# Kernel tuning notes

Hardware: AMD Instinct MI355X
Metric: run time of the kernel (lower is better)

## Reference

```python
import jax, jax.numpy as jnp
import numpy as np

B = 2048; E = 6; H = 4; D = 128; DH = D // H
LTXT = 24; CS = 20; JD = 7; SD = 16; LD = 32; K = 2
NLB = 4; NLD = 3; VOCAB = 512; DFF = 4 * D


def _ln(x, s, b, eps=1e-5):
    m = x.mean(-1, keepdims=True)
    v = ((x - m) ** 2).mean(-1, keepdims=True)
    return (x - m) * jax.lax.rsqrt(v + eps) * s + b


def _mha(xq, xkv, Wqkv, bqkv, Wo, bo, key_pad=None):
    # torch nn.MultiheadAttention, batch_first, eval (no dropout)
    Wq, Wk, Wv = jnp.split(Wqkv, 3, axis=-1)
    bq, bk, bv = jnp.split(bqkv, 3)
    Bc, Lq, _ = xq.shape
    Lk = xkv.shape[1]
    q = (xq @ Wq + bq).reshape(Bc, Lq, H, DH)
    k = (xkv @ Wk + bk).reshape(Bc, Lk, H, DH)
    v = (xkv @ Wv + bv).reshape(Bc, Lk, H, DH)
    s = jnp.einsum('bqhd,bkhd->bhqk', q, k) * (1.0 / DH ** 0.5)
    if key_pad is not None:
        s = jnp.where(key_pad[:, None, None, :], -1e9, s)
    a = jax.nn.softmax(s, axis=-1)
    o = jnp.einsum('bhqk,bkhd->bqhd', a, v).reshape(Bc, Lq, D)
    return o @ Wo + bo


def _sinusoidal_pe(L, d):
    pos = jnp.arange(L, dtype=jnp.float32)[:, None]
    div = jnp.exp(jnp.arange(0, d, 2, dtype=jnp.float32) * (-np.log(10000.0) / d))
    pe = jnp.zeros((L, d), jnp.float32)
    pe = pe.at[:, 0::2].set(jnp.sin(pos * div))
    return pe.at[:, 1::2].set(jnp.cos(pos * div))


def _forward(ids, state, tok_emb, pos_emb, bert_Wqkv, bert_bqkv, bert_Wo, bert_bo, bert_W1, bert_b1, bert_W2, bert_b2, bert_ln_s, bert_ln_b, bert_lnf_s, bert_lnf_b, se_W1, se_b1, se_W2, se_b2, se_ln_s, se_ln_b, r_W1, r_b1, r_W2, r_b2, r_ln_s, r_ln_b, gate_W, gate_b, exp_sp_W, exp_sp_b, exp_zp_W, exp_zp_b, exp_attn_Wqkv, exp_attn_bqkv, exp_attn_Wo, exp_attn_bo, exp_ln_s, exp_ln_b, exp_ff_W1, exp_ff_b1, exp_ff_W2, exp_ff_b2, exp_head_W, exp_head_b):
    Bc = ids.shape[0]
    gelu = lambda t: jax.nn.gelu(t, approximate=False)
    # ---- MiniBERT (post-LN encoder) ----
    pad = ids == 0  # PAD token
    x = tok_emb[ids] + pos_emb[None]  # [B,24,128]
    for l in range(NLB):
        a = _mha(x, x, bert_Wqkv[l], bert_bqkv[l], bert_Wo[l], bert_bo[l], pad)
        x = _ln(x + a, bert_ln_s[l, 0], bert_ln_b[l, 0])
        h = gelu(x @ bert_W1[l] + bert_b1[l]) @ bert_W2[l] + bert_b2[l]
        x = _ln(x + h, bert_ln_s[l, 1], bert_ln_b[l, 1])
    intent = _ln(x, bert_lnf_s, bert_lnf_b)[:, 0]  # CLS embedding [B,128]
    # ---- StateEncoder (MLP + LN) ----
    semb = _ln(gelu(state @ se_W1 + se_b1) @ se_W2 + se_b2, se_ln_s, se_ln_b)
    # ---- FusionRouter: top-k gating ----
    fused = _ln(gelu(jnp.concatenate([intent, semb], -1) @ r_W1 + r_b1) @ r_W2 + r_b2, r_ln_s, r_ln_b)
    logits = fused @ gate_W + gate_b  # [B,6]
    all_probs = jax.nn.softmax(logits, axis=-1)
    tv, ti = jax.lax.top_k(logits, K)
    weights = jax.nn.softmax(tv, axis=-1)  # [B,2]
    # ---- ACTExperts, inference path (z = 0) ----
    qpe = _sinusoidal_pe(CS, D)
    z = jnp.zeros((Bc, LD), state.dtype)

    def one_expert(sp_W, sp_b, zp_W, zp_b, aW, ab, oW, ob, lns, lnb, fW1, fb1, fW2, fb2, hW, hb):
        mem = jnp.stack([state @ sp_W + sp_b, z @ zp_W + zp_b], axis=1)  # [B,2,128]
        xq = jnp.broadcast_to(qpe[None], (Bc, CS, D))
        for l in range(NLD):  # norm_first decoder layers, relu FFN
            xn = _ln(xq, lns[l, 0], lnb[l, 0])
            xq = xq + _mha(xn, xn, aW[l, 0], ab[l, 0], oW[l, 0], ob[l, 0])
            xn = _ln(xq, lns[l, 1], lnb[l, 1])
            xq = xq + _mha(xn, mem, aW[l, 1], ab[l, 1], oW[l, 1], ob[l, 1])
            xn = _ln(xq, lns[l, 2], lnb[l, 2])
            xq = xq + jax.nn.relu(xn @ fW1[l] + fb1[l]) @ fW2[l] + fb2[l]
        return xq @ hW + hb  # [B,20,7]

    outs = jax.vmap(one_expert)(exp_sp_W, exp_sp_b, exp_zp_W, exp_zp_b, exp_attn_Wqkv, exp_attn_bqkv, exp_attn_Wo, exp_attn_bo, exp_ln_s, exp_ln_b, exp_ff_W1, exp_ff_b1, exp_ff_W2, exp_ff_b2, exp_head_W, exp_head_b)  # [E,B,20,7]
    # scatter top-k weights to a dense [B,E] gate and combine expert outputs
    w_full = jnp.zeros((Bc, E), logits.dtype).at[jnp.arange(Bc)[:, None], ti].add(weights)
    return jnp.einsum('be,ebtj->btj', w_full, outs)


def setup_inputs() -> dict:
    key = jax.random.key(0)
    it = iter(jax.random.split(key, 64))
    w = lambda *shape: jax.random.normal(next(it), shape, jnp.float32) * 0.05
    inp = {}
    inp['ids'] = jax.random.randint(next(it), (B, LTXT), 0, VOCAB, dtype=jnp.int32)
    inp['state'] = jax.random.normal(next(it), (B, SD), jnp.float32)
    inp['tok_emb'] = w(VOCAB, D).at[0].set(0.0)  # padding_idx=0
    inp['pos_emb'] = w(LTXT, D)
    inp['bert_Wqkv'] = w(NLB, D, 3 * D); inp['bert_bqkv'] = jnp.zeros((NLB, 3 * D))
    inp['bert_Wo'] = w(NLB, D, D); inp['bert_bo'] = jnp.zeros((NLB, D))
    inp['bert_W1'] = w(NLB, D, DFF); inp['bert_b1'] = jnp.zeros((NLB, DFF))
    inp['bert_W2'] = w(NLB, DFF, D); inp['bert_b2'] = jnp.zeros((NLB, D))
    inp['bert_ln_s'] = jnp.ones((NLB, 2, D)); inp['bert_ln_b'] = jnp.zeros((NLB, 2, D))
    inp['bert_lnf_s'] = jnp.ones((D,)); inp['bert_lnf_b'] = jnp.zeros((D,))
    inp['se_W1'] = w(SD, D); inp['se_b1'] = jnp.zeros((D,))
    inp['se_W2'] = w(D, D); inp['se_b2'] = jnp.zeros((D,))
    inp['se_ln_s'] = jnp.ones((D,)); inp['se_ln_b'] = jnp.zeros((D,))
    inp['r_W1'] = w(2 * D, D); inp['r_b1'] = jnp.zeros((D,))
    inp['r_W2'] = w(D, D); inp['r_b2'] = jnp.zeros((D,))
    inp['r_ln_s'] = jnp.ones((D,)); inp['r_ln_b'] = jnp.zeros((D,))
    inp['gate_W'] = w(D, E) * 10.0  # non-degenerate routing (source inits zeros)
    inp['gate_b'] = jnp.zeros((E,))
    inp['exp_sp_W'] = w(E, SD, D); inp['exp_sp_b'] = jnp.zeros((E, D))
    inp['exp_zp_W'] = w(E, LD, D); inp['exp_zp_b'] = jnp.zeros((E, D))
    inp['exp_attn_Wqkv'] = w(E, NLD, 2, D, 3 * D); inp['exp_attn_bqkv'] = jnp.zeros((E, NLD, 2, 3 * D))
    inp['exp_attn_Wo'] = w(E, NLD, 2, D, D); inp['exp_attn_bo'] = jnp.zeros((E, NLD, 2, D))
    inp['exp_ln_s'] = jnp.ones((E, NLD, 3, D)); inp['exp_ln_b'] = jnp.zeros((E, NLD, 3, D))
    inp['exp_ff_W1'] = w(E, NLD, D, DFF); inp['exp_ff_b1'] = jnp.zeros((E, NLD, DFF))
    inp['exp_ff_W2'] = w(E, NLD, DFF, D); inp['exp_ff_b2'] = jnp.zeros((E, NLD, D))
    inp['exp_head_W'] = w(E, D, JD); inp['exp_head_b'] = jnp.zeros((E, JD))
    return inp


def reference(ids, state, tok_emb, pos_emb, bert_Wqkv, bert_bqkv, bert_Wo, bert_bo, bert_W1, bert_b1, bert_W2, bert_b2, bert_ln_s, bert_ln_b, bert_lnf_s, bert_lnf_b, se_W1, se_b1, se_W2, se_b2, se_ln_s, se_ln_b, r_W1, r_b1, r_W2, r_b2, r_ln_s, r_ln_b, gate_W, gate_b, exp_sp_W, exp_sp_b, exp_zp_W, exp_zp_b, exp_attn_Wqkv, exp_attn_bqkv, exp_attn_Wo, exp_attn_bo, exp_ln_s, exp_ln_b, exp_ff_W1, exp_ff_b1, exp_ff_W2, exp_ff_b2, exp_head_W, exp_head_b):
    return _forward(ids, state, tok_emb, pos_emb, bert_Wqkv, bert_bqkv, bert_Wo, bert_bo, bert_W1, bert_b1, bert_W2, bert_b2, bert_ln_s, bert_ln_b, bert_lnf_s, bert_lnf_b, se_W1, se_b1, se_W2, se_b2, se_ln_s, se_ln_b, r_W1, r_b1, r_W2, r_b2, r_ln_s, r_ln_b, gate_W, gate_b, exp_sp_W, exp_sp_b, exp_zp_W, exp_zp_b, exp_attn_Wqkv, exp_attn_bqkv, exp_attn_Wo, exp_attn_bo, exp_ln_s, exp_ln_b, exp_ff_W1, exp_ff_b1, exp_ff_W2, exp_ff_b2, exp_head_W, exp_head_b)
```

## Files before the change

kernel.cpp:

```cpp
#include <hip/hip_runtime.h>
#include <math.h>

#define DEVI __device__ __forceinline__

namespace {

constexpr int Bn   = 2048;
constexpr int En   = 6;
constexpr int Hn   = 4;
constexpr int Dn   = 128;
constexpr int DHn  = 32;
constexpr int LTn  = 24;
constexpr int CSn  = 20;
constexpr int JDn  = 7;
constexpr int SDn  = 16;
constexpr int NLBn = 4;
constexpr int NLDn = 3;
constexpr int DFFn = 512;
constexpr float INV_SQRT_DH = 0.17677669529663687f;

constexpr int PAIRS  = 4096;
constexpr int MPMAX  = PAIRS * 20 + En * 128;
constexpr int NBGMAX = PAIRS * 20 / 128 + En;
constexpr int GEXP_OFF = 64;
constexpr int GMT_OFF  = 64 + NBGMAX;

constexpr int ROWSB = Bn * LTn;

constexpr int HSTR = 36;

typedef float f32x4v __attribute__((ext_vector_type(4)));
typedef short short8 __attribute__((ext_vector_type(8)));

DEVI float geluf(float x) { return 0.5f * x * (1.0f + erff(x * 0.70710678118654752f)); }

DEVI short f2bf(float f) {
  unsigned u = __float_as_uint(f);
  return (short)((u + 0x7FFFu + ((u >> 16) & 1u)) >> 16);
}
DEVI float bf2f(short s) { return __uint_as_float(((unsigned)(unsigned short)s) << 16); }
DEVI void split2(float v, short& h, short& l) {
  h = f2bf(v);
  l = f2bf(v - bf2f(h));
}

DEVI size_t apos(int row, int col, int KT) {
  return (((size_t)(row >> 4) * KT + (col >> 5)) * 64 + ((col >> 3) & 3) * 16 + (row & 15)) * 8
         + (col & 7);
}

DEVI size_t hpos(int rl, int col) {
  return (((size_t)((rl >> 4) * 16 + (col >> 5)) * 64) + ((col >> 3) & 3) * 16 + (rl & 15)) * 8
         + (col & 7);
}

__global__ void pack_kernel(const float* __restrict__ W, short* __restrict__ out,
                            const int K, const int N, const int total)
{
  const int p = (int)blockIdx.x * 256 + (int)threadIdx.x;
  if (p >= total) return;
  const int perMat = (K * N) >> 3;
  const int m = p / perMat, r = p - m * perMat;
  const int t = r >> 6, lane = r & 63;
  const int KT = K >> 5;
  const int nt = t / KT, kt = t - nt * KT;
  const int row0 = kt * 32 + (lane >> 4) * 8;
  const int col  = nt * 16 + (lane & 15);
  const float* src = W + (size_t)m * K * N;
  short8 v;
#pragma unroll
  for (int j = 0; j < 8; ++j) v[j] = f2bf(src[(size_t)(row0 + j) * N + col]);
  *reinterpret_cast<short8*>(out + (size_t)p * 8) = v;
}

__global__ void pack2_kernel(const float* __restrict__ W, short* __restrict__ out,
                             const int K, const int N, const int total)
{
  const int p = (int)blockIdx.x * 256 + (int)threadIdx.x;
  if (p >= total) return;
  const int perMat = (K * N) >> 3;
  const int m = p / perMat, r = p - m * perMat;
  const int t = r >> 6, lane = r & 63;
  const int KT = K >> 5;
  const int nt = t / KT, kt = t - nt * KT;
  const int row0 = kt * 32 + (lane >> 4) * 8;
  const int col  = nt * 16 + (lane & 15);
  const float* src = W + (size_t)m * K * N;
  short8 vh, vl;
// ... 117 lines not shown
    }
    acc *= INV_SQRT_DH;
    if (pad_s[j]) acc = -1e9f;
    att[e] = acc;
  }
  __syncthreads();
  if (tid < 2 * LTn) {
    const int r = tid >> 1, h0 = (tid & 1) * 12;
    float* row = att + r * LTn + h0;
    float m = row[0];
#pragma unroll
    for (int j = 1; j < 12; ++j) m = fmaxf(m, row[j]);
    m = fmaxf(m, __shfl_xor(m, 1));
    float s = 0.f;
#pragma unroll
    for (int j = 0; j < 12; ++j) { const float ex = expf(row[j] - m); row[j] = ex; s += ex; }
    s += __shfl_xor(s, 1);
    if ((tid & 1) == 0) inv[r] = 1.f / s;
  }
  __syncthreads();
  for (int e = tid; e < LTn * 32; e += 64) {
    const int i = e >> 5, c = e & 31;
    const float* arow = att + i * LTn;
    float acc = 0.f;
#pragma unroll 4
    for (int j = 0; j < LTn; ++j) acc = fmaf(arow[j], vs[j * HSTR + c], acc);
    acc *= inv[i];
    short hh, ll; split2(acc, hh, ll);
    const size_t pk = apos(row0 + i, h * 32 + c, 4);
    Ah[pk] = hh; Al[pk] = ll;
  }
}

__global__ __launch_bounds__(256) void bo_ln_kernel(
    const short* __restrict__ Ah, const short* __restrict__ Al,
    const short* __restrict__ Bp, const float* __restrict__ bo,
    const float* __restrict__ gs, const float* __restrict__ gb,
    float* __restrict__ X, short* __restrict__ OAh, short* __restrict__ OAl)
{
  __shared__ float red[16][4][2];
  const int mt0 = (int)blockIdx.x * 4;
  const int lane = (int)threadIdx.x & 63, wv = (int)threadIdx.x >> 6;
  const int r0 = lane & 15, g = lane >> 4;
  short8 bh[2][4], bl[2][4];
#pragma unroll
  for (int i = 0; i < 2; ++i)
#pragma unroll
    for (int kt = 0; kt < 4; ++kt) {
      const short* tb = Bp + (((size_t)(wv * 2 + i) * 4 + kt) << 10);
      bh[i][kt] = *reinterpret_cast<const short8*>(tb + lane * 8);
      bl[i][kt] = *reinterpret_cast<const short8*>(tb + 512 + lane * 8);
    }
  for (int mt = 0; mt < 4; ++mt) {
    const int mtg = mt0 + mt;
    short8 ah[4], al[4];
#pragma unroll
    for (int kt = 0; kt < 4; ++kt) {
      ah[kt] = *reinterpret_cast<const short8*>(Ah + (((size_t)mtg * 4 + kt) * 64 + lane) * 8);
      al[kt] = *reinterpret_cast<const short8*>(Al + (((size_t)mtg * 4 + kt) * 64 + lane) * 8);
    }
    float v[2][4];
#pragma unroll
    for (int i = 0; i < 2; ++i) {
      f32x4v c = {0.f, 0.f, 0.f, 0.f};
#pragma unroll
      for (int kt = 0; kt < 4; ++kt) {
        c = __builtin_amdgcn_mfma_f32_16x16x32_bf16(ah[kt], bh[i][kt], c, 0, 0, 0);
        c = __builtin_amdgcn_mfma_f32_16x16x32_bf16(al[kt], bh[i][kt], c, 0, 0, 0);
        c = __builtin_amdgcn_mfma_f32_16x16x32_bf16(ah[kt], bl[i][kt], c, 0, 0, 0);
      }
      const int col = (wv * 2 + i) * 16 + r0;
      const float bb = bo[col];
#pragma unroll
      for (int q = 0; q < 4; ++q) {
        const int row = mtg * 16 + g * 4 + q;
        v[i][q] = c[q] + bb + X[(size_t)row * 128 + col];
      }
    }
    float s1[4], s2[4];
#pragma unroll
    for (int q = 0; q < 4; ++q) {
      s1[q] = v[0][q] + v[1][q];
      s2[q] = v[0][q] * v[0][q] + v[1][q] * v[1][q];
    }
#pragma unroll
    for (int o = 1; o < 16; o <<= 1)
#pragma unroll
      for (int q = 0; q < 4; ++q) { s1[q] += __shfl_xor(s1[q], o); s2[q] += __shfl_xor(s2[q], o); }
    if (r0 == 0)
#pragma unroll
      for (int q = 0; q < 4; ++q) { red[g * 4 + q][wv][0] = s1[q]; red[g * 4 + q][wv][1] = s2[q]; }
    __syncthreads();
#pragma unroll
    for (int q = 0; q < 4; ++q) {
      const int r = g * 4 + q;
      const float t1 = red[r][0][0] + red[r][1][0] + red[r][2][0] + red[r][3][0];
      const float t2 = red[r][0][1] + red[r][1][1] + red[r][2][1] + red[r][3][1];
      const float m  = t1 * (1.f / 128.f);
      const float rs = rsqrtf(t2 * (1.f / 128.f) - m * m + 1e-5f);
      const int row = mtg * 16 + r;
#pragma unroll
      for (int i = 0; i < 2; ++i) {
        const int col = (wv * 2 + i) * 16 + r0;
        const float o = (v[i][q] - m) * rs * gs[col] + gb[col];
        X[(size_t)row * 128 + col] = o;
        short hh, ll; split2(o, hh, ll);
        const size_t pk = apos(row, col, 4);
        OAh[pk] = hh; OAl[pk] = ll;
      }
    }
    __syncthreads();
  }
}

__global__ __launch_bounds__(512) void bffn_kernel(
    const short* __restrict__ Ah, const short* __restrict__ Al,
    const short* __restrict__ W1p, const short* __restrict__ W2p,
    const float* __restrict__ b1, const float* __restrict__ b2,
    const float* __restrict__ gs, const float* __restrict__ gb,
    float* __restrict__ X, short* __restrict__ OAh, short* __restrict__ OAl)
{
  __shared__ short HhL[2 * 16 * 64 * 8];
  __shared__ short HlL[2 * 16 * 64 * 8];
  __shared__ float red[16][8][2];
  const int mtg0 = (int)blockIdx.x * 2;
  const int lane = (int)threadIdx.x & 63, wv = (int)threadIdx.x >> 6;
  const int r0 = lane & 15, g = lane >> 4;
  short8 ah[2][4], al[2][4];
#pragma unroll
  for (int mtl = 0; mtl < 2; ++mtl)
#pragma unroll
    for (int kt = 0; kt < 4; ++kt) {
      ah[mtl][kt] = *reinterpret_cast<const short8*>(
          Ah + (((size_t)(mtg0 + mtl) * 4 + kt) * 64 + lane) * 8);
      al[mtl][kt] = *reinterpret_cast<const short8*>(
          Al + (((size_t)(mtg0 + mtl) * 4 + kt) * 64 + lane) * 8);
    }
#pragma unroll
  for (int i = 0; i < 4; ++i) {
    const int nt = wv * 4 + i;
    short8 bh[4], bl[4];
#pragma unroll
    for (int kt = 0; kt < 4; ++kt) {
      const short* tb = W1p + (((size_t)(nt * 4 + kt)) << 10);
      bh[kt] = *reinterpret_cast<const short8*>(tb + lane * 8);
      bl[kt] = *reinterpret_cast<const short8*>(tb + 512 + lane * 8);
    }
    const int col = nt * 16 + r0;
    const float bb = b1[col];
#pragma unroll
    for (int mtl = 0; mtl < 2; ++mtl) {
      f32x4v c = {0.f, 0.f, 0.f, 0.f};
#pragma unroll
      for (int kt = 0; kt < 4; ++kt) {
        c = __builtin_amdgcn_mfma_f32_16x16x32_bf16(ah[mtl][kt], bh[kt], c, 0, 0, 0);
        c = __builtin_amdgcn_mfma_f32_16x16x32_bf16(al[mtl][kt], bh[kt], c, 0, 0, 0);
        c = __builtin_amdgcn_mfma_f32_16x16x32_bf16(ah[mtl][kt], bl[kt], c, 0, 0, 0);
      }
#pragma unroll
      for (int q = 0; q < 4; ++q) {
        const int rl = mtl * 16 + g * 4 + q;
        short hh, ll; split2(geluf(c[q] + bb), hh, ll);
        const size_t hp = hpos(rl, col);
        HhL[hp] = hh; HlL[hp] = ll;
      }
    }
  }
  __syncthreads();
  const int col = wv * 16 + r0;
  f32x4v c2[2];
#pragma unroll
  for (int mtl = 0; mtl < 2; ++mtl) c2[mtl] = (f32x4v){0.f, 0.f, 0.f, 0.f};
#pragma unroll
  for (int kk = 0; kk < 16; ++kk) {
    const short* tb = W2p + (((size_t)(wv * 16 + kk)) << 10);
    const short8 b2h = *reinterpret_cast<const short8*>(tb + lane * 8);
    const short8 b2l = *reinterpret_cast<const short8*>(tb + 512 + lane * 8);
#pragma unroll
    for (int mtl = 0; mtl < 2; ++mtl) {
      const size_t ap = (((size_t)(mtl * 16 + kk) * 64 + lane)) * 8;
      const short8 a2h = *reinterpret_cast<const short8*>(HhL + ap);
      const short8 a2l = *reinterpret_cast<const short8*>(HlL + ap);
      c2[mtl] = __builtin_amdgcn_mfma_f32_16x16x32_bf16(a2h, b2h, c2[mtl], 0, 0, 0);
      c2[mtl] = __builtin_amdgcn_mfma_f32_16x16x32_bf16(a2l, b2h, c2[mtl], 0, 0, 0);
      c2[mtl] = __builtin_amdgcn_mfma_f32_16x16x32_bf16(a2h, b2l, c2[mtl], 0, 0, 0);
    }
  }
  const float bb2 = b2[col];
  for (int mtl = 0; mtl < 2; ++mtl) {
    const int mtg = mtg0 + mtl;
    float v[4], s1[4], s2[4];
#pragma unroll
    for (int q = 0; q < 4; ++q) {
      const int row = mtg * 16 + g * 4 + q;
      v[q] = c2[mtl][q] + bb2 + X[(size_t)row * 128 + col];
      s1[q] = v[q]; s2[q] = v[q] * v[q];
    }
#pragma unroll
    for (int o = 1; o < 16; o <<= 1)
#pragma unroll
      for (int q = 0; q < 4; ++q) { s1[q] += __shfl_xor(s1[q], o); s2[q] += __shfl_xor(s2[q], o); }
    if (r0 == 0)
#pragma unroll
      for (int q = 0; q < 4; ++q) { red[g * 4 + q][wv][0] = s1[q]; red[g * 4 + q][wv][1] = s2[q]; }
    __syncthreads();
#pragma unroll
    for (int q = 0; q < 4; ++q) {
      const int r = g * 4 + q;
      float t1 = 0.f, t2 = 0.f;
#pragma unroll
      for (int w = 0; w < 8; ++w) { t1 += red[r][w][0]; t2 += red[r][w][1]; }
      const float m  = t1 * (1.f / 128.f);
      const float rs = rsqrtf(t2 * (1.f / 128.f) - m * m + 1e-5f);
      const int row = mtg * 16 + r;
      const float o = (v[q] - m) * rs * gs[col] + gb[col];
      X[(size_t)row * 128 + col] = o;
      short hh, ll; split2(o, hh, ll);
      const size_t pk = apos(row, col, 4);
      OAh[pk] = hh; OAl[pk] = ll;
    }
    __syncthreads();
  }
}

__global__ __launch_bounds__(256) void bintent_kernel(
    const float* __restrict__ X, const float* __restrict__ lnf_s,
    const float* __restrict__ lnf_b, float* __restrict__ intent)
{
  const int w = (int)threadIdx.x >> 6, lane = (int)threadIdx.x & 63;
  const int b = (int)blockIdx.x * 4 + w;
  const float* xr = X + (size_t)b * LTn * 128;
  const float a0 = xr[lane], a1 = xr[lane + 64];
  float s1 = a0 + a1, s2 = a0 * a0 + a1 * a1;
#pragma unroll
  for (int o = 32; o > 0; o >>= 1) { s1 += __shfl_xor(s1, o); s2 += __shfl_xor(s2, o); }
  const float m  = s1 * (1.f / 128.f);
  const float rs = rsqrtf(s2 * (1.f / 128.f) - m * m + 1e-5f);
  intent[b * 128 + lane]      = (a0 - m) * rs * lnf_s[lane]      + lnf_b[lane];
  intent[b * 128 + lane + 64] = (a1 - m) * rs * lnf_s[lane + 64] + lnf_b[lane + 64];
}

struct RouterP {
  const float* state; const float* intent;
  const float* se_W1; const float* se_b1; const float* se_W2; const float* se_b2;
  const float* se_ln_s; const float* se_ln_b;
  const float* r_W1; const float* r_b1; const float* r_W2; const float* r_b2;
  const float* r_ln_s; const float* r_ln_b;
  const float* gate_W; const float* gate_b;
// ... 278 lines not shown
        for (int q = 0; q < 4; ++q) { red[g * 4 + q][wv][0] = s1[q]; red[g * 4 + q][wv][1] = s2[q]; }
      __syncthreads();
#pragma unroll
      for (int q = 0; q < 4; ++q) {
        const int r = g * 4 + q;
        const float t1 = red[r][0][0] + red[r][1][0] + red[r][2][0] + red[r][3][0];
        const float t2 = red[r][0][1] + red[r][1][1] + red[r][2][1] + red[r][3][1];
        const float m  = t1 * (1.f / 128.f);
        const float rs = rsqrtf(t2 * (1.f / 128.f) - m * m + 1e-5f);
        const int row = (mt0 + mt) * 16 + r;
#pragma unroll
        for (int i = 0; i < 2; ++i) {
          const int col = (wv * 2 + i) * 16 + r0;
          const float o = (v[i][q] - m) * rs * gs[col] + gb[col];
          X[(size_t)row * 128 + col] = v[i][q];
          OutP[apos(row, col, 4)] = f2bf(o);
        }
      }
      __syncthreads();
    }
  }
}

template<bool DOLN>
__global__ __launch_bounds__(512) void effn_kernel(
    const short* __restrict__ A, const short* __restrict__ W1b, const int strideW1,
    const float* __restrict__ b1b, const int strideB1,
    const short* __restrict__ W2b, const int strideW2,
    const float* __restrict__ b2b, const int strideB2,
    float* __restrict__ X, short* __restrict__ OutP,
    const float* __restrict__ lnsA, const float* __restrict__ lnbA, const int subOff,
    const int* __restrict__ sch)
{
  __shared__ short HsL[4 * 16 * 64 * 8];
  __shared__ float red[16][8][2];
  const int k = (int)blockIdx.x;
  if (k >= sch[0]) return;
  const int ex  = sch[GEXP_OFF + k];
  const int mt0 = sch[GMT_OFF + k] + (int)blockIdx.y * 4;
  const short* W1p = W1b + (size_t)ex * strideW1;
  const short* W2p = W2b + (size_t)ex * strideW2;
  const float* b1 = b1b + (size_t)ex * strideB1;
  const float* b2 = b2b + (size_t)ex * strideB2;
  const float* gs = DOLN ? lnsA + ex * (NLDn * 3 * 128) + subOff : nullptr;
  const float* gb = DOLN ? lnbA + ex * (NLDn * 3 * 128) + subOff : nullptr;
  const int lane = (int)threadIdx.x & 63, wv = (int)threadIdx.x >> 6;
  const int r0 = lane & 15, g = lane >> 4;
  short8 a[4][4];
#pragma unroll
  for (int mtl = 0; mtl < 4; ++mtl)
#pragma unroll
    for (int kt = 0; kt < 4; ++kt)
      a[mtl][kt] = *reinterpret_cast<const short8*>(
          A + (((size_t)(mt0 + mtl) * 4 + kt) * 64 + lane) * 8);
#pragma unroll
  for (int i = 0; i < 4; ++i) {
    const int nt = wv * 4 + i;
    short8 bw[4];
#pragma unroll
    for (int kt = 0; kt < 4; ++kt)
      bw[kt] = *reinterpret_cast<const short8*>(
          W1p + (((size_t)(nt * 4 + kt) * 64 + lane)) * 8);
    const int col = nt * 16 + r0;
    const float bb = b1[col];
#pragma unroll
    for (int mtl = 0; mtl < 4; ++mtl) {
      f32x4v c = {0.f, 0.f, 0.f, 0.f};
#pragma unroll
      for (int kt = 0; kt < 4; ++kt)
        c = __builtin_amdgcn_mfma_f32_16x16x32_bf16(a[mtl][kt], bw[kt], c, 0, 0, 0);
#pragma unroll
      for (int q = 0; q < 4; ++q) {
        const int rl = mtl * 16 + g * 4 + q;
        HsL[hpos(rl, col)] = f2bf(fmaxf(c[q] + bb, 0.f));
      }
    }
  }
  __syncthreads();
  const int col = wv * 16 + r0;
  f32x4v c2[4];
#pragma unroll
  for (int mtl = 0; mtl < 4; ++mtl) c2[mtl] = (f32x4v){0.f, 0.f, 0.f, 0.f};
#pragma unroll
  for (int kk = 0; kk < 16; ++kk) {
    const short8 bw = *reinterpret_cast<const short8*>(
        W2p + (((size_t)(wv * 16 + kk) * 64 + lane)) * 8);
#pragma unroll
    for (int mtl = 0; mtl < 4; ++mtl) {
      const short8 aw = *reinterpret_cast<const short8*>(
          HsL + (((size_t)(mtl * 16 + kk) * 64 + lane)) * 8);
      c2[mtl] = __builtin_amdgcn_mfma_f32_16x16x32_bf16(aw, bw, c2[mtl], 0, 0, 0);
    }
  }
  const float bb2 = b2[col];
  for (int mtl = 0; mtl < 4; ++mtl) {
    const int mtg = mt0 + mtl;
    float v[4];
#pragma unroll
    for (int q = 0; q < 4; ++q) {
      const int row = mtg * 16 + g * 4 + q;
      v[q] = c2[mtl][q] + bb2 + X[(size_t)row * 128 + col];
    }
    if (DOLN) {
      float s1[4], s2[4];
#pragma unroll
      for (int q = 0; q < 4; ++q) { s1[q] = v[q]; s2[q] = v[q] * v[q]; }
#pragma unroll
      for (int o = 1; o < 16; o <<= 1)
#pragma unroll
        for (int q = 0; q < 4; ++q) { s1[q] += __shfl_xor(s1[q], o); s2[q] += __shfl_xor(s2[q], o); }
      if (r0 == 0)
#pragma unroll
        for (int q = 0; q < 4; ++q) { red[g * 4 + q][wv][0] = s1[q]; red[g * 4 + q][wv][1] = s2[q]; }
      __syncthreads();
#pragma unroll
      for (int q = 0; q < 4; ++q) {
        const int r = g * 4 + q;
        float t1 = 0.f, t2 = 0.f;
#pragma unroll
        for (int w = 0; w < 8; ++w) { t1 += red[r][w][0]; t2 += red[r][w][1]; }
        const float m  = t1 * (1.f / 128.f);
        const float rs = rsqrtf(t2 * (1.f / 128.f) - m * m + 1e-5f);
        const int row = mtg * 16 + r;
        const float o = (v[q] - m) * rs * gs[col] + gb[col];
        X[(size_t)row * 128 + col] = v[q];
        OutP[apos(row, col, 4)] = f2bf(o);
// ... 249 lines not shown
    pack_kernel<<<dim3((t2c + 255) / 256), dim3(256), 0, stream>>>(
        (const float*)d_in[42], pF2, 512, 128, t2c);
    const int bq = 4 * 6144;
    pack2_kernel<<<dim3((bq + 255) / 256), dim3(256), 0, stream>>>(
        (const float*)d_in[4], pbQ, 128, 384, bq);
    const int bo = 4 * 2048;
    pack2_kernel<<<dim3((bo + 255) / 256), dim3(256), 0, stream>>>(
        (const float*)d_in[6], pbO, 128, 128, bo);
    const int bw1 = 4 * 8192;
    pack2_kernel<<<dim3((bw1 + 255) / 256), dim3(256), 0, stream>>>(
        (const float*)d_in[8], pbW1, 128, 512, bw1);
    const int bw2 = 4 * 8192;
    pack2_kernel<<<dim3((bw2 + 255) / 256), dim3(256), 0, stream>>>(
        (const float*)d_in[10], pbW2, 512, 128, bw2);
    compose_kernel<<<dim3(En * NLDn), dim3(256), 0, stream>>>(
        (const float*)d_in[30], (const float*)d_in[31], (const float*)d_in[33],
        (const float*)d_in[34], (const float*)d_in[35], Cmat, k0c, k1c);
  }

  {
    const float* bq  = (const float*)d_in[5];
    const float* bo  = (const float*)d_in[7];
    const float* b1  = (const float*)d_in[9];
    const float* b2  = (const float*)d_in[11];
    const float* lns = (const float*)d_in[12];
    const float* lnb = (const float*)d_in[13];

    bembed_kernel<<<dim3(ROWSB / 16), dim3(256), 0, stream>>>(
        ids, tok_emb, pos_emb, Xb, Ah, Al);
    for (int l = 0; l < NLBn; ++l) {
      bqkv_kernel<<<dim3(ROWSB / 64, 3), dim3(256), 0, stream>>>(
          Ah, Al, pbQ + (size_t)l * 98304, bq + l * 384, SBb);
      battn_kernel<<<dim3(Bn, Hn), dim3(64), 0, stream>>>(SBb, ids, Ah, Al);
      bo_ln_kernel<<<dim3(ROWSB / 64), dim3(256), 0, stream>>>(
          Ah, Al, pbO + (size_t)l * 32768, bo + l * 128,
          lns + l * 256, lnb + l * 256, Xb, Ah, Al);
      bffn_kernel<<<dim3(ROWSB / 32), dim3(512), 0, stream>>>(
          Ah, Al, pbW1 + (size_t)l * 131072, pbW2 + (size_t)l * 131072,
          b1 + l * 512, b2 + l * 128,
          lns + l * 256 + 128, lnb + l * 256 + 128, Xb, Ah, Al);
    }
    bintent_kernel<<<dim3(Bn / 4), dim3(256), 0, stream>>>(
        Xb, (const float*)d_in[14], (const float*)d_in[15], intent);
  }

  {
    RouterP rp;
    rp.state = state; rp.intent = intent;
    rp.se_W1 = (const float*)d_in[16]; rp.se_b1 = (const float*)d_in[17];
    rp.se_W2 = (const float*)d_in[18]; rp.se_b2 = (const float*)d_in[19];
    rp.se_ln_s = (const float*)d_in[20]; rp.se_ln_b = (const float*)d_in[21];
    rp.r_W1 = (const float*)d_in[22]; rp.r_b1 = (const float*)d_in[23];
    rp.r_W2 = (const float*)d_in[24]; rp.r_b2 = (const float*)d_in[25];
    rp.r_ln_s = (const float*)d_in[26]; rp.r_ln_b = (const float*)d_in[27];
    rp.gate_W = (const float*)d_in[28]; rp.gate_b = (const float*)d_in[29];
    rp.ridx = ridx; rp.rwgt = rwgt;
    router_kernel<<<dim3(Bn), dim3(128), 0, stream>>>(rp);
  }

  const float* ab   = (const float*)d_in[35];
  const float* abo  = (const float*)d_in[37];
  const float* lnsA = (const float*)d_in[38];
  const float* lnbA = (const float*)d_in[39];
  const float* fb1A = (const float*)d_in[41];
  const float* fb2A = (const float*)d_in[43];
  const float* hW   = (const float*)d_in[44];
  const float* hB   = (const float*)d_in[45];

  {
    sched_kernel<<<dim3(1), dim3(256), 0, stream>>>(ridx, sch, plist, prow, pexp, ppos);
    xinit_kernel<<<dim3(MPMAX * 32 / 256), dim3(256), 0, stream>>>(qpe, sch, X2);
    ln_pack_kernel<<<dim3(MPMAX / 16), dim3(256), 0, stream>>>(
        X2, ANP, lnsA, lnbA, 0, sch);
// ... 39 lines not shown
```

Before: 1.410 ms.

## Fuse attention output projection, LayerNorm and FFN into one BERT kernel

Merges the output-projection+LayerNorm kernel and the FFN+LayerNorm kernel into a single 512-thread kernel per 32-row tile. The normalized attention output is kept in LDS as a bf16 hi/lo split instead of round-tripping through global X and the packed A buffers. The FFN hidden layer is computed in two halves to fit LDS, which adds extra barriers. This removes one launch per layer and a global write/read of the intermediate activations. The second residual is now rebuilt from the split bf16 copy, giving a slightly different rounding path.

```diff
diff --git a/kernel.cpp b/kernel.cpp
--- a/kernel.cpp
+++ b/kernel.cpp
@@ -54,6 +54,11 @@
          + (col & 7);
 }
 
+DEVI size_t hposh(int rl, int col) {
+  return (((size_t)((rl >> 4) * 8 + (col >> 5)) * 64) + ((col >> 3) & 3) * 16 + (rl & 15)) * 8
+         + (col & 7);
+}
+
 __global__ void pack_kernel(const float* __restrict__ W, short* __restrict__ out,
                             const int K, const int N, const int total)
 {
@@ -237,168 +242,151 @@
   }
 }
 
-__global__ __launch_bounds__(256) void bo_ln_kernel(
+__global__ __launch_bounds__(512) void bfused_kernel(
     const short* __restrict__ Ah, const short* __restrict__ Al,
-    const short* __restrict__ Bp, const float* __restrict__ bo,
-    const float* __restrict__ gs, const float* __restrict__ gb,
-    float* __restrict__ X, short* __restrict__ OAh, short* __restrict__ OAl)
-{
-  __shared__ float red[16][4][2];
-  const int mt0 = (int)blockIdx.x * 4;
-  const int lane = (int)threadIdx.x & 63, wv = (int)threadIdx.x >> 6;
-  const int r0 = lane & 15, g = lane >> 4;
-  short8 bh[2][4], bl[2][4];
-#pragma unroll
-  for (int i = 0; i < 2; ++i)
-#pragma unroll
-    for (int kt = 0; kt < 4; ++kt) {
-      const short* tb = Bp + (((size_t)(wv * 2 + i) * 4 + kt) << 10);
-      bh[i][kt] = *reinterpret_cast<const short8*>(tb + lane * 8);
-      bl[i][kt] = *reinterpret_cast<const short8*>(tb + 512 + lane * 8);
-    }
-  for (int mt = 0; mt < 4; ++mt) {
-    const int mtg = mt0 + mt;
-    short8 ah[4], al[4];
-#pragma unroll
-    for (int kt = 0; kt < 4; ++kt) {
-      ah[kt] = *reinterpret_cast<const short8*>(Ah + (((size_t)mtg * 4 + kt) * 64 + lane) * 8);
-      al[kt] = *reinterpret_cast<const short8*>(Al + (((size_t)mtg * 4 + kt) * 64 + lane) * 8);
-    }
-    float v[2][4];
-#pragma unroll
-    for (int i = 0; i < 2; ++i) {
-      f32x4v c = {0.f, 0.f, 0.f, 0.f};
-#pragma unroll
-      for (int kt = 0; kt < 4; ++kt) {
-        c = __builtin_amdgcn_mfma_f32_16x16x32_bf16(ah[kt], bh[i][kt], c, 0, 0, 0);
-        c = __builtin_amdgcn_mfma_f32_16x16x32_bf16(al[kt], bh[i][kt], c, 0, 0, 0);
-        c = __builtin_amdgcn_mfma_f32_16x16x32_bf16(ah[kt], bl[i][kt], c, 0, 0, 0);
-      }
-      const int col = (wv * 2 + i) * 16 + r0;
-      const float bb = bo[col];
-#pragma unroll
-      for (int q = 0; q < 4; ++q) {
-        const int row = mtg * 16 + g * 4 + q;
-        v[i][q] = c[q] + bb + X[(size_t)row * 128 + col];
-      }
-    }
-    float s1[4], s2[4];
-#pragma unroll
-    for (int q = 0; q < 4; ++q) {
-      s1[q] = v[0][q] + v[1][q];
-      s2[q] = v[0][q] * v[0][q] + v[1][q] * v[1][q];
-    }
-#pragma unroll
-    for (int o = 1; o < 16; o <<= 1)
-#pragma unroll
-      for (int q = 0; q < 4; ++q) { s1[q] += __shfl_xor(s1[q], o); s2[q] += __shfl_xor(s2[q], o); }
-    if (r0 == 0)
-#pragma unroll
-      for (int q = 0; q < 4; ++q) { red[g * 4 + q][wv][0] = s1[q]; red[g * 4 + q][wv][1] = s2[q]; }
-    __syncthreads();
-#pragma unroll
-    for (int q = 0; q < 4; ++q) {
-      const int r = g * 4 + q;
-      const float t1 = red[r][0][0] + red[r][1][0] + red[r][2][0] + red[r][3][0];
-      const float t2 = red[r][0][1] + red[r][1][1] + red[r][2][1] + red[r][3][1];
-      const float m  = t1 * (1.f / 128.f);
-      const float rs = rsqrtf(t2 * (1.f / 128.f) - m * m + 1e-5f);
-      const int row = mtg * 16 + r;
-#pragma unroll
-      for (int i = 0; i < 2; ++i) {
-        const int col = (wv * 2 + i) * 16 + r0;
-        const float o = (v[i][q] - m) * rs * gs[col] + gb[col];
-        X[(size_t)row * 128 + col] = o;
-        short hh, ll; split2(o, hh, ll);
-        const size_t pk = apos(row, col, 4);
-        OAh[pk] = hh; OAl[pk] = ll;
-      }
-    }
-    __syncthreads();
-  }
-}
-
-__global__ __launch_bounds__(512) void bffn_kernel(
-    const short* __restrict__ Ah, const short* __restrict__ Al,
+    const short* __restrict__ Op, const float* __restrict__ bo,
+    const float* __restrict__ gs1, const float* __restrict__ gb1,
     const short* __restrict__ W1p, const short* __restrict__ W2p,
     const float* __restrict__ b1, const float* __restrict__ b2,
-    const float* __restrict__ gs, const float* __restrict__ gb,
+    const float* __restrict__ gs2, const float* __restrict__ gb2,
     float* __restrict__ X, short* __restrict__ OAh, short* __restrict__ OAl)
 {
-  __shared__ short HhL[2 * 16 * 64 * 8];
-  __shared__ short HlL[2 * 16 * 64 * 8];
+  __shared__ short AhL[2 * 4 * 64 * 8];
+  __shared__ short AlL[2 * 4 * 64 * 8];
+  __shared__ short HhL[2 * 8 * 64 * 8];
+  __shared__ short HlL[2 * 8 * 64 * 8];
   __shared__ float red[16][8][2];
   const int mtg0 = (int)blockIdx.x * 2;
   const int lane = (int)threadIdx.x & 63, wv = (int)threadIdx.x >> 6;
   const int r0 = lane & 15, g = lane >> 4;
-  short8 ah[2][4], al[2][4];
-#pragma unroll
-  for (int mtl = 0; mtl < 2; ++mtl)
+  const int col = wv * 16 + r0;
+
+  float vA[2][4];
+  {
+    short8 obh[4], obl[4];
 #pragma unroll
     for (int kt = 0; kt < 4; ++kt) {
-      ah[mtl][kt] = *reinterpret_cast<const short8*>(
-          Ah + (((size_t)(mtg0 + mtl) * 4 + kt) * 64 + lane) * 8);
-      al[mtl][kt] = *reinterpret_cast<const short8*>(
-          Al + (((size_t)(mtg0 + mtl) * 4 + kt) * 64 + lane) * 8);
-    }
-#pragma unroll
-  for (int i = 0; i < 4; ++i) {
-    const int nt = wv * 4 + i;
-    short8 bh[4], bl[4];
-#pragma unroll
-    for (int kt = 0; kt < 4; ++kt) {
-      const short* tb = W1p + (((size_t)(nt * 4 + kt)) << 10);
-      bh[kt] = *reinterpret_cast<const short8*>(tb + lane * 8);
-      bl[kt] = *reinterpret_cast<const short8*>(tb + 512 + lane * 8);
-    }
-    const int col = nt * 16 + r0;
-    const float bb = b1[col];
+      const short* tb = Op + (((size_t)(wv * 4 + kt)) << 10);
+      obh[kt] = *reinterpret_cast<const short8*>(tb + lane * 8);
+      obl[kt] = *reinterpret_cast<const short8*>(tb + 512 + lane * 8);
+    }
+    const float bbo = bo[col];
 #pragma unroll
     for (int mtl = 0; mtl < 2; ++mtl) {
+      const int mtg = mtg0 + mtl;
       f32x4v c = {0.f, 0.f, 0.f, 0.f};
 #pragma unroll
       for (int kt = 0; kt < 4; ++kt) {
-        c = __builtin_amdgcn_mfma_f32_16x16x32_bf16(ah[mtl][kt], bh[kt], c, 0, 0, 0);
-        c = __builtin_amdgcn_mfma_f32_16x16x32_bf16(al[mtl][kt], bh[kt], c, 0, 0, 0);
-        c = __builtin_amdgcn_mfma_f32_16x16x32_bf16(ah[mtl][kt], bl[kt], c, 0, 0, 0);
+        const short8 ah = *reinterpret_cast<const short8*>(
+            Ah + (((size_t)mtg * 4 + kt) * 64 + lane) * 8);
+        const short8 al = *reinterpret_cast<const short8*>(
+            Al + (((size_t)mtg * 4 + kt) * 64 + lane) * 8);
+        c = __builtin_amdgcn_mfma_f32_16x16x32_bf16(ah, obh[kt], c, 0, 0, 0);
+        c = __builtin_amdgcn_mfma_f32_16x16x32_bf16(al, obh[kt], c, 0, 0, 0);
+        c = __builtin_amdgcn_mfma_f32_16x16x32_bf16(ah, obl[kt], c, 0, 0, 0);
       }
 #pragma unroll
       for (int q = 0; q < 4; ++q) {
-        const int rl = mtl * 16 + g * 4 + q;
-        short hh, ll; split2(geluf(c[q] + bb), hh, ll);
-        const size_t hp = hpos(rl, col);
-        HhL[hp] = hh; HlL[hp] = ll;
-      }
-    }
-  }
-  __syncthreads();
-  const int col = wv * 16 + r0;
+        const int row = mtg * 16 + g * 4 + q;
+        vA[mtl][q] = c[q] + bbo + X[(size_t)row * 128 + col];
+      }
+    }
+  }
+  for (int mtl = 0; mtl < 2; ++mtl) {
+    float s1[4], s2[4];
+#pragma unroll
+    for (int q = 0; q < 4; ++q) { s1[q] = vA[mtl][q]; s2[q] = vA[mtl][q] * vA[mtl][q]; }
+#pragma unroll
+    for (int o = 1; o < 16; o <<= 1)
+#pragma unroll
+      for (int q = 0; q < 4; ++q) { s1[q] += __shfl_xor(s1[q], o); s2[q] += __shfl_xor(s2[q], o); }
+    if (r0 == 0)
+#pragma unroll
+      for (int q = 0; q < 4; ++q) { red[g * 4 + q][wv][0] = s1[q]; red[g * 4 + q][wv][1] = s2[q]; }
+    __syncthreads();
+#pragma unroll
+    for (int q = 0; q < 4; ++q) {
+      const int r = g * 4 + q;
+      float t1 = 0.f, t2 = 0.f;
+#pragma unroll
+      for (int w = 0; w < 8; ++w) { t1 += red[r][w][0]; t2 += red[r][w][1]; }
+      const float m  = t1 * (1.f / 128.f);
+      const float rs = rsqrtf(t2 * (1.f / 128.f) - m * m + 1e-5f);
+      const float o = (vA[mtl][q] - m) * rs * gs1[col] + gb1[col];
+      short hh, ll; split2(o, hh, ll);
+      const size_t pk = apos(mtl * 16 + r, col, 4);
+      AhL[pk] = hh; AlL[pk] = ll;
+    }
+    __syncthreads();
+  }
+
   f32x4v c2[2];
 #pragma unroll
   for (int mtl = 0; mtl < 2; ++mtl) c2[mtl] = (f32x4v){0.f, 0.f, 0.f, 0.f};
-#pragma unroll
-  for (int kk = 0; kk < 16; ++kk) {
-    const short* tb = W2p + (((size_t)(wv * 16 + kk)) << 10);
-    const short8 b2h = *reinterpret_cast<const short8*>(tb + lane * 8);
-    const short8 b2l = *reinterpret_cast<const short8*>(tb + 512 + lane * 8);
-#pragma unroll
-    for (int mtl = 0; mtl < 2; ++mtl) {
-      const size_t ap = (((size_t)(mtl * 16 + kk) * 64 + lane)) * 8;
-      const short8 a2h = *reinterpret_cast<const short8*>(HhL + ap);
-      const short8 a2l = *reinterpret_cast<const short8*>(HlL + ap);
-      c2[mtl] = __builtin_amdgcn_mfma_f32_16x16x32_bf16(a2h, b2h, c2[mtl], 0, 0, 0);
-      c2[mtl] = __builtin_amdgcn_mfma_f32_16x16x32_bf16(a2l, b2h, c2[mtl], 0, 0, 0);
-      c2[mtl] = __builtin_amdgcn_mfma_f32_16x16x32_bf16(a2h, b2l, c2[mtl], 0, 0, 0);
-    }
-  }
+  for (int half = 0; half < 2; ++half) {
+    if (half) __syncthreads();
+#pragma unroll
+    for (int i = 0; i < 2; ++i) {
+      const int ntl = wv * 2 + i;
+      const int ntg = half * 16 + ntl;
+      short8 bh[4], bl[4];
+#pragma unroll
+      for (int kt = 0; kt < 4; ++kt) {
+        const short* tb = W1p + (((size_t)(ntg * 4 + kt)) << 10);
+        bh[kt] = *reinterpret_cast<const short8*>(tb + lane * 8);
+        bl[kt] = *reinterpret_cast<const short8*>(tb + 512 + lane * 8);
+      }
+      const int colh = ntl * 16 + r0;
+      const float bb = b1[ntg * 16 + r0];
+#pragma unroll
+      for (int mtl = 0; mtl < 2; ++mtl) {
+        f32x4v c = {0.f, 0.f, 0.f, 0.f};
+#pragma unroll
+        for (int kt = 0; kt < 4; ++kt) {
+          const size_t ap = (((size_t)(mtl * 4 + kt) * 64 + lane)) * 8;
+          const short8 a2h = *reinterpret_cast<const short8*>(AhL + ap);
+          const short8 a2l = *reinterpret_cast<const short8*>(AlL + ap);
+          c = __builtin_amdgcn_mfma_f32_16x16x32_bf16(a2h, bh[kt], c, 0, 0, 0);
+          c = __builtin_amdgcn_mfma_f32_16x16x32_bf16(a2l, bh[kt], c, 0, 0, 0);
+          c = __builtin_amdgcn_mfma_f32_16x16x32_bf16(a2h, bl[kt], c, 0, 0, 0);
+        }
+#pragma unroll
+        for (int q = 0; q < 4; ++q) {
+          const int rl = mtl * 16 + g * 4 + q;
+          short hh, ll; split2(geluf(c[q] + bb), hh, ll);
+          const size_t hp = hposh(rl, colh);
+          HhL[hp] = hh; HlL[hp] = ll;
+        }
+      }
+    }
+    __syncthreads();
+#pragma unroll
+    for (int kk = 0; kk < 8; ++kk) {
+      const int kkg = half * 8 + kk;
+      const short* tb = W2p + (((size_t)(wv * 16 + kkg)) << 10);
+      const short8 b2h = *reinterpret_cast<const short8*>(tb + lane * 8);
+      const short8 b2l = *reinterpret_cast<const short8*>(tb + 512 + lane * 8);
+#pragma unroll
+      for (int mtl = 0; mtl < 2; ++mtl) {
+        const size_t ap = (((size_t)(mtl * 8 + kk) * 64 + lane)) * 8;
+        const short8 a2h = *reinterpret_cast<const short8*>(HhL + ap);
+        const short8 a2l = *reinterpret_cast<const short8*>(HlL + ap);
+        c2[mtl] = __builtin_amdgcn_mfma_f32_16x16x32_bf16(a2h, b2h, c2[mtl], 0, 0, 0);
+        c2[mtl] = __builtin_amdgcn_mfma_f32_16x16x32_bf16(a2l, b2h, c2[mtl], 0, 0, 0);
+        c2[mtl] = __builtin_amdgcn_mfma_f32_16x16x32_bf16(a2h, b2l, c2[mtl], 0, 0, 0);
+      }
+    }
+  }
+  __syncthreads();
   const float bb2 = b2[col];
   for (int mtl = 0; mtl < 2; ++mtl) {
     const int mtg = mtg0 + mtl;
     float v[4], s1[4], s2[4];
 #pragma unroll
     for (int q = 0; q < 4; ++q) {
-      const int row = mtg * 16 + g * 4 + q;
-      v[q] = c2[mtl][q] + bb2 + X[(size_t)row * 128 + col];
+      const size_t pk = apos(mtl * 16 + g * 4 + q, col, 4);
+      const float oatt = bf2f(AhL[pk]) + bf2f(AlL[pk]);
+      v[q] = c2[mtl][q] + bb2 + oatt;
       s1[q] = v[q]; s2[q] = v[q] * v[q];
     }
 #pragma unroll
@@ -418,7 +406,7 @@
       const float m  = t1 * (1.f / 128.f);
       const float rs = rsqrtf(t2 * (1.f / 128.f) - m * m + 1e-5f);
       const int row = mtg * 16 + r;
-      const float o = (v[q] - m) * rs * gs[col] + gb[col];
+      const float o = (v[q] - m) * rs * gs2[col] + gb2[col];
       X[(size_t)row * 128 + col] = o;
       short hh, ll; split2(o, hh, ll);
       const size_t pk = apos(row, col, 4);
@@ -1138,13 +1126,13 @@
       bqkv_kernel<<<dim3(ROWSB / 64, 3), dim3(256), 0, stream>>>(
           Ah, Al, pbQ + (size_t)l * 98304, bq + l * 384, SBb);
       battn_kernel<<<dim3(Bn, Hn), dim3(64), 0, stream>>>(SBb, ids, Ah, Al);
-      bo_ln_kernel<<<dim3(ROWSB / 64), dim3(256), 0, stream>>>(
+      bfused_kernel<<<dim3(ROWSB / 32), dim3(512), 0, stream>>>(
           Ah, Al, pbO + (size_t)l * 32768, bo + l * 128,
-          lns + l * 256, lnb + l * 256, Xb, Ah, Al);
-      bffn_kernel<<<dim3(ROWSB / 32), dim3(512), 0, stream>>>(
-          Ah, Al, pbW1 + (size_t)l * 131072, pbW2 + (size_t)l * 131072,
+          lns + l * 256, lnb + l * 256,
+          pbW1 + (size_t)l * 131072, pbW2 + (size_t)l * 131072,
           b1 + l * 512, b2 + l * 128,
-          lns + l * 256 + 128, lnb + l * 256 + 128, Xb, Ah, Al);
+          lns + l * 256 + 128, lnb + l * 256 + 128,
+          Xb, Ah, Al);
     }
     bintent_kernel<<<dim3(Bn / 4), dim3(256), 0, stream>>>(
         Xb, (const float*)d_in[14], (const float*)d_in[15], intent);
```

Result: slower. 1.520 ms (+7.8%).

## Split FFN hidden dimension into two halves to halve LDS footprint

Applied to the files above, without the earlier changes.

Both the BERT FFN and expert FFN kernels now process the 512-wide hidden layer in two 256-wide halves. Each half computes its GELU/ReLU activations into shared memory, then immediately accumulates the second GEMM over that half. This halves the LDS buffers, which can let more blocks reside per CU. The cost is an extra barrier per half and reloading the A fragments once per half.

```diff
diff --git a/kernel.cpp b/kernel.cpp
--- a/kernel.cpp
+++ b/kernel.cpp
@@ -49,8 +49,8 @@
          + (col & 7);
 }
 
-DEVI size_t hpos(int rl, int col) {
-  return (((size_t)((rl >> 4) * 16 + (col >> 5)) * 64) + ((col >> 3) & 3) * 16 + (rl & 15)) * 8
+DEVI size_t hposh(int rl, int col) {
+  return (((size_t)((rl >> 4) * 8 + (col >> 5)) * 64) + ((col >> 3) & 3) * 16 + (rl & 15)) * 8
          + (col & 7);
 }
 
@@ -325,72 +325,80 @@
     const float* __restrict__ gs, const float* __restrict__ gb,
     float* __restrict__ X, short* __restrict__ OAh, short* __restrict__ OAl)
 {
-  __shared__ short HhL[2 * 16 * 64 * 8];
-  __shared__ short HlL[2 * 16 * 64 * 8];
+  __shared__ short HhL[2 * 8 * 64 * 8];
+  __shared__ short HlL[2 * 8 * 64 * 8];
   __shared__ float red[16][8][2];
   const int mtg0 = (int)blockIdx.x * 2;
   const int lane = (int)threadIdx.x & 63, wv = (int)threadIdx.x >> 6;
   const int r0 = lane & 15, g = lane >> 4;
-  short8 ah[2][4], al[2][4];
-#pragma unroll
-  for (int mtl = 0; mtl < 2; ++mtl)
-#pragma unroll
-    for (int kt = 0; kt < 4; ++kt) {
-      ah[mtl][kt] = *reinterpret_cast<const short8*>(
-          Ah + (((size_t)(mtg0 + mtl) * 4 + kt) * 64 + lane) * 8);
-      al[mtl][kt] = *reinterpret_cast<const short8*>(
-          Al + (((size_t)(mtg0 + mtl) * 4 + kt) * 64 + lane) * 8);
-    }
-#pragma unroll
-  for (int i = 0; i < 4; ++i) {
-    const int nt = wv * 4 + i;
-    short8 bh[4], bl[4];
-#pragma unroll
-    for (int kt = 0; kt < 4; ++kt) {
-      const short* tb = W1p + (((size_t)(nt * 4 + kt)) << 10);
-      bh[kt] = *reinterpret_cast<const short8*>(tb + lane * 8);
-      bl[kt] = *reinterpret_cast<const short8*>(tb + 512 + lane * 8);
-    }
-    const int col = nt * 16 + r0;
-    const float bb = b1[col];
-#pragma unroll
-    for (int mtl = 0; mtl < 2; ++mtl) {
-      f32x4v c = {0.f, 0.f, 0.f, 0.f};
-#pragma unroll
-      for (int kt = 0; kt < 4; ++kt) {
-        c = __builtin_amdgcn_mfma_f32_16x16x32_bf16(ah[mtl][kt], bh[kt], c, 0, 0, 0);
-        c = __builtin_amdgcn_mfma_f32_16x16x32_bf16(al[mtl][kt], bh[kt], c, 0, 0, 0);
-        c = __builtin_amdgcn_mfma_f32_16x16x32_bf16(ah[mtl][kt], bl[kt], c, 0, 0, 0);
-      }
-#pragma unroll
-      for (int q = 0; q < 4; ++q) {
-        const int rl = mtl * 16 + g * 4 + q;
-        short hh, ll; split2(geluf(c[q] + bb), hh, ll);
-        const size_t hp = hpos(rl, col);
-        HhL[hp] = hh; HlL[hp] = ll;
-      }
-    }
-  }
-  __syncthreads();
+  f32x4v c2[2];
+  c2[0] = (f32x4v){0.f, 0.f, 0.f, 0.f};
+  c2[1] = (f32x4v){0.f, 0.f, 0.f, 0.f};
+#pragma unroll 1
+  for (int half = 0; half < 2; ++half) {
+    if (half) __syncthreads();
+    {
+      short8 ah[2][4], al[2][4];
+#pragma unroll
+      for (int mtl = 0; mtl < 2; ++mtl)
+#pragma unroll
+        for (int kt = 0; kt < 4; ++kt) {
+          ah[mtl][kt] = *reinterpret_cast<const short8*>(
+              Ah + (((size_t)(mtg0 + mtl) * 4 + kt) * 64 + lane) * 8);
+          al[mtl][kt] = *reinterpret_cast<const short8*>(
+              Al + (((size_t)(mtg0 + mtl) * 4 + kt) * 64 + lane) * 8);
+        }
+#pragma unroll
+      for (int i = 0; i < 2; ++i) {
+        const int ntl = wv * 2 + i;
+        const int ntg = half * 16 + ntl;
+        short8 bh[4], bl[4];
+#pragma unroll
+        for (int kt = 0; kt < 4; ++kt) {
+          const short* tb = W1p + (((size_t)(ntg * 4 + kt)) << 10);
+          bh[kt] = *reinterpret_cast<const short8*>(tb + lane * 8);
+          bl[kt] = *reinterpret_cast<const short8*>(tb + 512 + lane * 8);
+        }
+        const int colh = ntl * 16 + r0;
+        const float bb = b1[ntg * 16 + r0];
+#pragma unroll
+        for (int mtl = 0; mtl < 2; ++mtl) {
+          f32x4v c = {0.f, 0.f, 0.f, 0.f};
+#pragma unroll
+          for (int kt = 0; kt < 4; ++kt) {
+            c = __builtin_amdgcn_mfma_f32_16x16x32_bf16(ah[mtl][kt], bh[kt], c, 0, 0, 0);
+            c = __builtin_amdgcn_mfma_f32_16x16x32_bf16(al[mtl][kt], bh[kt], c, 0, 0, 0);
+            c = __builtin_amdgcn_mfma_f32_16x16x32_bf16(ah[mtl][kt], bl[kt], c, 0, 0, 0);
+          }
+#pragma unroll
+          for (int q = 0; q < 4; ++q) {
+            const int rl = mtl * 16 + g * 4 + q;
+            short hh, ll; split2(geluf(c[q] + bb), hh, ll);
+            const size_t hp = hposh(rl, colh);
+            HhL[hp] = hh; HlL[hp] = ll;
+          }
+        }
+      }
+    }
+    __syncthreads();
+#pragma unroll
+    for (int kk = 0; kk < 8; ++kk) {
+      const int kkg = half * 8 + kk;
+      const short* tb = W2p + (((size_t)(wv * 16 + kkg)) << 10);
+      const short8 b2h = *reinterpret_cast<const short8*>(tb + lane * 8);
+      const short8 b2l = *reinterpret_cast<const short8*>(tb + 512 + lane * 8);
+#pragma unroll
+      for (int mtl = 0; mtl < 2; ++mtl) {
+        const size_t ap = (((size_t)(mtl * 8 + kk) * 64 + lane)) * 8;
+        const short8 a2h = *reinterpret_cast<const short8*>(HhL + ap);
+        const short8 a2l = *reinterpret_cast<const short8*>(HlL + ap);
+        c2[mtl] = __builtin_amdgcn_mfma_f32_16x16x32_bf16(a2h, b2h, c2[mtl], 0, 0, 0);
+        c2[mtl] = __builtin_amdgcn_mfma_f32_16x16x32_bf16(a2l, b2h, c2[mtl], 0, 0, 0);
+        c2[mtl] = __builtin_amdgcn_mfma_f32_16x16x32_bf16(a2h, b2l, c2[mtl], 0, 0, 0);
+      }
+    }
+  }
   const int col = wv * 16 + r0;
-  f32x4v c2[2];
-#pragma unroll
-  for (int mtl = 0; mtl < 2; ++mtl) c2[mtl] = (f32x4v){0.f, 0.f, 0.f, 0.f};
-#pragma unroll
-  for (int kk = 0; kk < 16; ++kk) {
-    const short* tb = W2p + (((size_t)(wv * 16 + kk)) << 10);
-    const short8 b2h = *reinterpret_cast<const short8*>(tb + lane * 8);
-    const short8 b2l = *reinterpret_cast<const short8*>(tb + 512 + lane * 8);
-#pragma unroll
-    for (int mtl = 0; mtl < 2; ++mtl) {
-      const size_t ap = (((size_t)(mtl * 16 + kk) * 64 + lane)) * 8;
-      const short8 a2h = *reinterpret_cast<const short8*>(HhL + ap);
-      const short8 a2l = *reinterpret_cast<const short8*>(HlL + ap);
-      c2[mtl] = __builtin_amdgcn_mfma_f32_16x16x32_bf16(a2h, b2h, c2[mtl], 0, 0, 0);
-      c2[mtl] = __builtin_amdgcn_mfma_f32_16x16x32_bf16(a2l, b2h, c2[mtl], 0, 0, 0);
-      c2[mtl] = __builtin_amdgcn_mfma_f32_16x16x32_bf16(a2h, b2l, c2[mtl], 0, 0, 0);
-    }
-  }
   const float bb2 = b2[col];
   for (int mtl = 0; mtl < 2; ++mtl) {
     const int mtg = mtg0 + mtl;
@@ -763,7 +771,7 @@
     const float* __restrict__ lnsA, const float* __restrict__ lnbA, const int subOff,
     const int* __restrict__ sch)
 {
-  __shared__ short HsL[4 * 16 * 64 * 8];
+  __shared__ short HsL[4 * 8 * 64 * 8];
   __shared__ float red[16][8][2];
   const int k = (int)blockIdx.x;
   if (k >= sch[0]) return;
@@ -777,52 +785,60 @@
   const float* gb = DOLN ? lnbA + ex * (NLDn * 3 * 128) + subOff : nullptr;
   const int lane = (int)threadIdx.x & 63, wv = (int)threadIdx.x >> 6;
   const int r0 = lane & 15, g = lane >> 4;
-  short8 a[4][4];
-#pragma unroll
-  for (int mtl = 0; mtl < 4; ++mtl)
-#pragma unroll
-    for (int kt = 0; kt < 4; ++kt)
-      a[mtl][kt] = *reinterpret_cast<const short8*>(
-          A + (((size_t)(mt0 + mtl) * 4 + kt) * 64 + lane) * 8);
-#pragma unroll
-  for (int i = 0; i < 4; ++i) {
-    const int nt = wv * 4 + i;
-    short8 bw[4];
-#pragma unroll
-    for (int kt = 0; kt < 4; ++kt)
-      bw[kt] = *reinterpret_cast<const short8*>(
-          W1p + (((size_t)(nt * 4 + kt) * 64 + lane)) * 8);
-    const int col = nt * 16 + r0;
-    const float bb = b1[col];
-#pragma unroll
-    for (int mtl = 0; mtl < 4; ++mtl) {
-      f32x4v c = {0.f, 0.f, 0.f, 0.f};
-#pragma unroll
-      for (int kt = 0; kt < 4; ++kt)
-        c = __builtin_amdgcn_mfma_f32_16x16x32_bf16(a[mtl][kt], bw[kt], c, 0, 0, 0);
-#pragma unroll
-      for (int q = 0; q < 4; ++q) {
-        const int rl = mtl * 16 + g * 4 + q;
-        HsL[hpos(rl, col)] = f2bf(fmaxf(c[q] + bb, 0.f));
-      }
-    }
-  }
-  __syncthreads();
+  f32x4v c2[4];
+#pragma unroll
+  for (int mtl = 0; mtl < 4; ++mtl) c2[mtl] = (f32x4v){0.f, 0.f, 0.f, 0.f};
+#pragma unroll 1
+  for (int half = 0; half < 2; ++half) {
+    if (half) __syncthreads();
+    {
+      short8 a[4][4];
+#pragma unroll
+      for (int mtl = 0; mtl < 4; ++mtl)
+#pragma unroll
+        for (int kt = 0; kt < 4; ++kt)
+          a[mtl][kt] = *reinterpret_cast<const short8*>(
+              A + (((size_t)(mt0 + mtl) * 4 + kt) * 64 + lane) * 8);
+#pragma unroll
+      for (int i = 0; i < 2; ++i) {
+        const int ntl = wv * 2 + i;
+        const int ntg = half * 16 + ntl;
+        short8 bw[4];
+#pragma unroll
+        for (int kt = 0; kt < 4; ++kt)
+          bw[kt] = *reinterpret_cast<const short8*>(
+              W1p + (((size_t)(ntg * 4 + kt) * 64 + lane)) * 8);
+        const int colh = ntl * 16 + r0;
+        const float bb = b1[ntg * 16 + r0];
+#pragma unroll
+        for (int mtl = 0; mtl < 4; ++mtl) {
+          f32x4v c = {0.f, 0.f, 0.f, 0.f};
+#pragma unroll
+          for (int kt = 0; kt < 4; ++kt)
+            c = __builtin_amdgcn_mfma_f32_16x16x32_bf16(a[mtl][kt], bw[kt], c, 0, 0, 0);
+#pragma unroll
+          for (int q = 0; q < 4; ++q) {
+            const int rl = mtl * 16 + g * 4 + q;
+            HsL[hposh(rl, colh)] = f2bf(fmaxf(c[q] + bb, 0.f));
+          }
+        }
+      }
+    }
+    __syncthreads();
+#pragma unroll
+    for (int kk = 0; kk < 8; ++kk) {
+      const int kkg = half * 8 + kk;
+      const short8 bw = *reinterpret_cast<const short8*>(
+          W2p + (((size_t)(wv * 16 + kkg) * 64 + lane)) * 8);
+#pragma unroll
+      for (int mtl = 0; mtl < 4; ++mtl) {
+        const short8 aw = *reinterpret_cast<const short8*>(
+            HsL + (((size_t)(mtl * 8 + kk) * 64 + lane)) * 8);
+        c2[mtl] = __builtin_amdgcn_mfma_f32_16x16x32_bf16(aw, bw, c2[mtl], 0, 0, 0);
+      }
+    }
+  }
   const int col = wv * 16 + r0;
-  f32x4v c2[4];
-#pragma unroll
-  for (int mtl = 0; mtl < 4; ++mtl) c2[mtl] = (f32x4v){0.f, 0.f, 0.f, 0.f};
-#pragma unroll
-  for (int kk = 0; kk < 16; ++kk) {
-    const short8 bw = *reinterpret_cast<const short8*>(
-        W2p + (((size_t)(wv * 16 + kk) * 64 + lane)) * 8);
-#pragma unroll
-    for (int mtl = 0; mtl < 4; ++mtl) {
-      const short8 aw = *reinterpret_cast<const short8*>(
-          HsL + (((size_t)(mtl * 16 + kk) * 64 + lane)) * 8);
-      c2[mtl] = __builtin_amdgcn_mfma_f32_16x16x32_bf16(aw, bw, c2[mtl], 0, 0, 0);
-    }
-  }
   const float bb2 = b2[col];
   for (int mtl = 0; mtl < 4; ++mtl) {
     const int mtg = mt0 + mtl;
```

New measurement: 1.552 ms. 10.0% more time.
